# Kernel optimization log

Measured on AMD Instinct MI355X. Metric: run time of the kernel, lower is better.

Reference implementation:

```python
import jax, jax.numpy as jnp
import numpy as np

C = 128      # out_channels
G = 4        # RecConvLayer num_groups
BS, CIN, H, W = 4, 3, 96, 96
GN = 8
EPS = 1e-5


def _conv2d(x, w, b, pad):
    out = jax.lax.conv_general_dilated(
        x, w, (1, 1), [(pad, pad), (pad, pad)],
        dimension_numbers=("NCHW", "OIHW", "NCHW"))
    return out + b[None, :, None, None]


def _prelu(x, a):
    return jnp.maximum(x, 0) + a[0] * jnp.minimum(x, 0)


def _group_norm(x, w, b):
    bs, c, h, wd = x.shape
    xg = x.reshape(bs, GN, c // GN, h, wd)
    mu = xg.mean(axis=(2, 3, 4), keepdims=True)
    var = xg.var(axis=(2, 3, 4), keepdims=True)  # biased, as torch GroupNorm
    xn = ((xg - mu) * jax.lax.rsqrt(var + EPS)).reshape(bs, c, h, wd)
    return xn * w[None, :, None, None] + b[None, :, None, None]


def _single_conv(x, w, b, a, gw, gb, pad):
    # SingleConvLayer in eval mode: Conv2d -> PReLU -> GroupNorm (no noise)
    return _group_norm(_prelu(_conv2d(x, w, b, pad), a), gw, gb)


def _bidir_gru_layer(x, wih, whh, bih, bhh):
    # x: (T,B,Din); wih: (2,3C,Din); whh: (2,3C,C); bih/bhh: (2,3C)
    Cc = whh.shape[-1]
    h0 = jnp.zeros((x.shape[1], Cc), x.dtype)

    def run_dir(gx, wh, bh):
        def step(h, g):
            gh = h @ wh.T + bh
            r = jax.nn.sigmoid(g[:, :Cc] + gh[:, :Cc])
            z = jax.nn.sigmoid(g[:, Cc:2 * Cc] + gh[:, Cc:2 * Cc])
            n = jnp.tanh(g[:, 2 * Cc:] + r * gh[:, 2 * Cc:])
            hn = (1.0 - z) * n + z * h
            return hn, hn
        return jax.lax.scan(step, h0, gx)[1]

    yf = run_dir(x @ wih[0].T + bih[0], whh[0], bhh[0])
    yb = run_dir(x[::-1] @ wih[1].T + bih[1], whh[1], bhh[1])[::-1]
    return jnp.concatenate([yf, yb], axis=-1)  # (T,B,2C)


def _gru2(x, wih0, whh0, bih0, bhh0, wih1, whh1, bih1, bhh1):
    y = _bidir_gru_layer(x, wih0, whh0, bih0, bhh0)
    return _bidir_gru_layer(y, wih1, whh1, bih1, bhh1)


_gru_groups = jax.vmap(_gru2, in_axes=(1, 0, 0, 0, 0, 0, 0, 0, 0), out_axes=1)


def _run_gru(x_tgbc, p):
    out = _gru_groups(x_tgbc, *p)               # (T,G,B,2C)
    t, g, b, _ = out.shape
    return out.reshape(t, g, b, 2, -1).mean(axis=3)  # mean over directions -> (T,G,B,C)


def _forward(x, conv1_w, conv1_b, prelu1_a, gn1_w, gn1_b,
             conv2_w, conv2_b, prelu2_a, gn2_w, gn2_b,
             comb_w, comb_b, prelu3_a, gn3_w, gn3_b,
             h_wih0, h_whh0, h_bih0, h_bhh0, h_wih1, h_whh1, h_bih1, h_bhh1,
             v_wih0, v_whh0, v_bih0, v_bhh0, v_wih1, v_whh1, v_bih1, v_bhh1,
             h1_wih0, h1_whh0, h1_bih0, h1_bhh0, h1_wih1, h1_whh1, h1_bih1, h1_bhh1,
             v1_wih0, v1_whh0, v1_bih0, v1_bhh0, v1_wih1, v1_whh1, v1_bih1, v1_bhh1):
    x = _single_conv(x, conv1_w, conv1_b, prelu1_a, gn1_w, gn1_b, 1)
    x = _single_conv(x, conv2_w, conv2_b, prelu2_a, gn2_w, gn2_b, 1)
    bs, c, m, n = x.shape
    vg, hg = n // G, m // G
    y = jnp.transpose(x, (0, 3, 2, 1))                               # (bs,n,m,c)
    y1 = jnp.transpose(y.reshape(bs, G, vg * m, c), (2, 1, 0, 3))    # vertical seqs (m*vg,G,bs,c)
    ym = jnp.transpose(y, (0, 2, 1, 3))                              # (bs,m,n,c)
    y2 = jnp.transpose(ym.reshape(bs, G, hg * n, c), (2, 1, 0, 3))   # horizontal seqs (n*hg,G,bs,c)

    hn = _run_gru(y2, (h_wih0, h_whh0, h_bih0, h_bhh0, h_wih1, h_whh1, h_bih1, h_bhh1))
    vn = _run_gru(y1, (v_wih0, v_whh0, v_bih0, v_bhh0, v_wih1, v_whh1, v_bih1, v_bhh1))

    hn_b = jnp.transpose(hn, (2, 1, 0, 3)).reshape(bs, m, n, c)
    y1b = jnp.transpose(jnp.transpose(hn_b, (0, 2, 1, 3)).reshape(bs, G, vg * m, c), (2, 1, 0, 3))
    vn_b = jnp.transpose(vn, (2, 1, 0, 3)).reshape(bs, n, m, c)
    y2b = jnp.transpose(jnp.transpose(vn_b, (0, 2, 1, 3)).reshape(bs, G, hg * n, c), (2, 1, 0, 3))

    hn2 = _run_gru(y2b, (h1_wih0, h1_whh0, h1_bih0, h1_bhh0, h1_wih1, h1_whh1, h1_bih1, h1_bhh1))
    vn2 = _run_gru(y1b, (v1_wih0, v1_whh0, v1_bih0, v1_bhh0, v1_wih1, v1_whh1, v1_bih1, v1_bhh1))

    hcnm = jnp.transpose(jnp.transpose(hn2, (2, 1, 0, 3)).reshape(bs, m, n, c), (0, 3, 1, 2))  # (bs,c,m,n)
    vcnm = jnp.transpose(jnp.transpose(vn2, (2, 1, 0, 3)).reshape(bs, n, m, c), (0, 3, 2, 1))  # (bs,c,m,n)
    return _single_conv(jnp.concatenate([hcnm, vcnm], axis=1), comb_w, comb_b, prelu3_a, gn3_w, gn3_b, 0)


def setup_inputs() -> dict:
    key = jax.random.key(0)
    ks = jax.random.split(key, 8)
    nrm = lambda k, s, sc: jax.random.normal(k, s, jnp.float32) * sc
    inp = {
        "x": nrm(ks[0], (BS, CIN, H, W), 1.0),
        "conv1_w": nrm(ks[1], (C, CIN, 3, 3), 0.1), "conv1_b": nrm(ks[2], (C,), 0.05),
        "prelu1_a": jnp.full((1,), 0.25, jnp.float32),
        "gn1_w": jnp.ones((C,), jnp.float32), "gn1_b": jnp.zeros((C,), jnp.float32),
        "conv2_w": nrm(ks[3], (C, C, 3, 3), 0.03), "conv2_b": nrm(ks[4], (C,), 0.05),
        "prelu2_a": jnp.full((1,), 0.25, jnp.float32),
        "gn2_w": jnp.ones((C,), jnp.float32), "gn2_b": jnp.zeros((C,), jnp.float32),
        "comb_w": nrm(ks[5], (C, 2 * C, 1, 1), 0.05), "comb_b": nrm(ks[6], (C,), 0.05),
        "prelu3_a": jnp.full((1,), 0.25, jnp.float32),
        "gn3_w": jnp.ones((C,), jnp.float32), "gn3_b": jnp.zeros((C,), jnp.float32),
    }
    shapes = [("wih0", (G, 2, 3 * C, C)), ("whh0", (G, 2, 3 * C, C)),
              ("bih0", (G, 2, 3 * C)), ("bhh0", (G, 2, 3 * C)),
              ("wih1", (G, 2, 3 * C, 2 * C)), ("whh1", (G, 2, 3 * C, C)),
              ("bih1", (G, 2, 3 * C)), ("bhh1", (G, 2, 3 * C))]
    for i, p in enumerate(["h", "v", "h1", "v1"]):
        kp = jax.random.split(jax.random.fold_in(key, 100 + i), 8)
        for j, (nm, sh) in enumerate(shapes):
            inp[p + "_" + nm] = nrm(kp[j], sh, 0.05)
    return inp


def reference(x, conv1_w, conv1_b, prelu1_a, gn1_w, gn1_b,
              conv2_w, conv2_b, prelu2_a, gn2_w, gn2_b,
              comb_w, comb_b, prelu3_a, gn3_w, gn3_b,
              h_wih0, h_whh0, h_bih0, h_bhh0, h_wih1, h_whh1, h_bih1, h_bhh1,
              v_wih0, v_whh0, v_bih0, v_bhh0, v_wih1, v_whh1, v_bih1, v_bhh1,
              h1_wih0, h1_whh0, h1_bih0, h1_bhh0, h1_wih1, h1_whh1, h1_bih1, h1_bhh1,
              v1_wih0, v1_whh0, v1_bih0, v1_bhh0, v1_wih1, v1_whh1, v1_bih1, v1_bhh1):
    return _forward(x, conv1_w, conv1_b, prelu1_a, gn1_w, gn1_b,
                    conv2_w, conv2_b, prelu2_a, gn2_w, gn2_b,
                    comb_w, comb_b, prelu3_a, gn3_w, gn3_b,
                    h_wih0, h_whh0, h_bih0, h_bhh0, h_wih1, h_whh1, h_bih1, h_bhh1,
                    v_wih0, v_whh0, v_bih0, v_bhh0, v_wih1, v_whh1, v_bih1, v_bhh1,
                    h1_wih0, h1_whh0, h1_bih0, h1_bhh0, h1_wih1, h1_whh1, h1_bih1, h1_bhh1,
                    v1_wih0, v1_whh0, v1_bih0, v1_bhh0, v1_wih1, v1_whh1, v1_bih1, v1_bhh1)
```

## Files before the change

kernel.cpp:

```cpp
#include <hip/hip_runtime.h>

typedef unsigned short u16;
typedef __attribute__((ext_vector_type(8))) short bf16x8;
typedef __attribute__((ext_vector_type(4))) float f32x4;
typedef __attribute__((ext_vector_type(4))) int   i32x4;

#define DEVFN static __device__ __forceinline__
#define AS_G __attribute__((address_space(1)))
#define AS_L __attribute__((address_space(3)))

DEVFN float b2f(u16 u){ return __uint_as_float(((unsigned int)u)<<16); }
DEVFN u16 f2b(float f){ unsigned int x = __float_as_uint(f); x += 0x7FFFu + ((x>>16)&1u); return (u16)(x>>16); }
DEVFN float fastrcp(float x){ return __builtin_amdgcn_rcpf(x); }

struct CastArgs { const float* s[8]; u16* d[8]; int n[8]; };
__global__ void castf2b_g(CastArgs a)
{
    int p = blockIdx.y;
    int i = blockIdx.x*256 + threadIdx.x;
    if (i < a.n[p]) a.d[p][i] = f2b(a.s[p][i]);
}

struct QuantArgs { const float* w[8]; char* q[8]; float* dq[8]; };
__global__ void quant_whh_g(QuantArgs a)
{
    int p = blockIdx.y;
    int row = blockIdx.x;
    int lane = threadIdx.x;
    const float* wr = a.w[p] + (long long)row*128;
    float v0 = wr[lane], v1 = wr[lane+64];
    float m = fmaxf(fabsf(v0), fabsf(v1));
#pragma unroll
    for (int off = 32; off; off >>= 1) m = fmaxf(m, __shfl_xor(m, off));
    float s = (m > 0.f) ? m * (1.f/127.f) : 1.f;
    float inv = 1.f / s;
    a.q[p][(long long)row*128 + lane]      = (char)__float2int_rn(v0 * inv);
    a.q[p][(long long)row*128 + lane + 64] = (char)__float2int_rn(v1 * inv);
    if (lane == 0) a.dq[p][row] = s * (1.f/127.f);
}

__global__ __launch_bounds__(256)
void gemm_bt(const u16* __restrict__ A, const u16* __restrict__ B,
             const float* __restrict__ bias, u16* __restrict__ C,
             int K, int N,
             long long zA, long long zB, long long zBias, long long zC,
             const float* __restrict__ alphaP, float* __restrict__ stats, int rowsPerB)
{
    __shared__ __align__(16) u16 As[128*32];
    __shared__ __align__(16) u16 Bs[128*32];
    __shared__ float sstat[16];

    const int tid  = threadIdx.x;
    const int wave = tid >> 6, lane = tid & 63;
    const int quad = lane >> 4, l16 = lane & 15;
    const int wm = wave & 1, wn = wave >> 1;
    const long long z = blockIdx.z;
    A += z * zA; B += z * zB; C += z * zC;
    if (bias) bias += z * zBias;
    const int lin   = blockIdx.y * gridDim.x + blockIdx.x;
    const int mBase = (int)(lin / gridDim.y) * 128;
    const int nBase = (int)(lin % gridDim.y) * 128;

    f32x4 acc[4][4];
#pragma unroll
    for (int i = 0; i < 4; i++)
#pragma unroll
        for (int j = 0; j < 4; j++) acc[i][j] = (f32x4){0.f,0.f,0.f,0.f};

    const int srow = lane >> 2;
    const int sk   = (lane & 3) * 8;
    const int nK = K >> 5;

    for (int kk = 0; kk < nK; ++kk) {
        const int k0 = kk << 5;
#pragma unroll
        for (int q = 0; q < 2; q++) {
            const u16* ga = A + (long long)(mBase + wave*32 + q*16 + srow) * K + k0 + sk;
            const u16* gb = B + (long long)(nBase + wave*32 + q*16 + srow) * K + k0 + sk;
            __builtin_amdgcn_global_load_lds((const AS_G unsigned int*)ga,
                (AS_L unsigned int*)(As + (wave*32 + q*16)*32), 16, 0, 0);
            __builtin_amdgcn_global_load_lds((const AS_G unsigned int*)gb,
                (AS_L unsigned int*)(Bs + (wave*32 + q*16)*32), 16, 0, 0);
        }
        __syncthreads();
        bf16x8 af[4], bfr[4];
#pragma unroll
        for (int mt = 0; mt < 4; mt++) af[mt]  = *(const bf16x8*)(As + (wm*64 + mt*16 + l16)*32 + quad*8);
#pragma unroll
        for (int nt = 0; nt < 4; nt++) bfr[nt] = *(const bf16x8*)(Bs + (wn*64 + nt*16 + l16)*32 + quad*8);
#pragma unroll
        for (int mt = 0; mt < 4; mt++)
#pragma unroll
            for (int nt = 0; nt < 4; nt++)
                acc[mt][nt] = __builtin_amdgcn_mfma_f32_16x16x32_bf16(af[mt], bfr[nt], acc[mt][nt], 0, 0, 0);
        __syncthreads();
    }

    const bool doStats = (stats != nullptr);
    const float alpha = alphaP ? alphaP[0] : 0.f;
    if (doStats) { if (tid < 16) sstat[tid] = 0.f; __syncthreads(); }

    float lsum[4] = {0,0,0,0}, lsq[4] = {0,0,0,0};
#pragma unroll
    for (int nt = 0; nt < 4; nt++) {
        const int col = nBase + wn*64 + nt*16 + l16;
        const float bv = bias ? bias[col] : 0.f;
#pragma unroll
        for (int mt = 0; mt < 4; mt++) {
#pragma unroll
            for (int r = 0; r < 4; r++) {
                const int row = mBase + wm*64 + mt*16 + quad*4 + r;
                float v = acc[mt][nt][r] + bv;
                if (alphaP) v = v > 0.f ? v : alpha * v;
                C[(long long)row * N + col] = f2b(v);
                lsum[nt] += v; lsq[nt] += v * v;
            }
        }
    }
    if (doStats) {
#pragma unroll
        for (int nt = 0; nt < 4; nt++) {
            const int gn = wn*4 + nt;
            atomicAdd(&sstat[gn], lsum[nt]);
            atomicAdd(&sstat[8 + gn], lsq[nt]);
        }
        __syncthreads();
        if (tid < 16) {
            const int b = mBase / rowsPerB;
            atomicAdd(&stats[b*16 + tid], sstat[tid]);
        }
    }
}

#define HSB 144
#define BURST 16
#define NCHUNK 16
#define CHUNK  144
#define WARM   112

__global__ __launch_bounds__(512, 2)
void gru_rec(const u16* __restrict__ gxH, const u16* __restrict__ gxV,
             const char* __restrict__ qwH, const char* __restrict__ qwV,
             const float* __restrict__ dqH, const float* __restrict__ dqV,
             const float* __restrict__ bhhH, const float* __restrict__ bhhV,
             u16* __restrict__ outH, u16* __restrict__ outV)
{
    const int id    = blockIdx.x / NCHUNK;
    const int chunk = blockIdx.x % NCHUNK;
    const int stack = id >> 3, g = (id >> 1) & 3, d = id & 1;
    const u16*  gx  = (stack ? gxV : gxH) + (long long)g*9216*768 + d*384;
    const char* qw  = (stack ? qwV : qwH) + (long long)(g*2 + d)*384*128;
    const float* dqv = (stack ? dqV : dqH) + (g*2 + d)*384;
    const float* bhh = (stack ? bhhV : bhhH) + (g*2 + d)*384;
    u16* out = (stack ? outV : outH) + (long long)g*9216*256 + d*128;

    const int sBegin = chunk * CHUNK;
    const int sEnd   = sBegin + CHUNK;
    const int sw     = (chunk == 0) ? 0 : sBegin - WARM;

    const int tid = threadIdx.x;
    const int w = tid >> 6, lane = tid & 63;
    const int quad = lane >> 4, l16 = lane & 15;

    __shared__ __align__(16) char hbf8[2][16*HSB];
    __shared__ __align__(16) u16 outs[2][BURST*512];
    for (int i = tid; i < 2*16*HSB; i += 512) ((char*)hbf8)[i] = 0;

    const int col = w*16 + l16;
    i32x4 ifrag[3][2];
#pragma unroll
    for (int gate = 0; gate < 3; ++gate)
#pragma unroll
        for (int kc = 0; kc < 2; ++kc)
            ifrag[gate][kc] = *(const i32x4*)(qw + (long long)(gate*128 + col)*128 + kc*64 + quad*16);

    const float dqR = dqv[col], dqZ = dqv[128 + col], dqN = dqv[256 + col];
    const float bhr = bhh[col], bhz = bhh[128 + col], bhn = bhh[256 + col];
    float h = 0.f;

    const int step = d ? -1 : 1;
    const int t0 = d ? 2303 : 0;
    const long long rowStride = (long long)step * 3072;

    u16 bankA[BURST][3], bankB[BURST][3];
    const i32x4 zi = {0,0,0,0};

    auto loadBank = [&](u16 (&bk)[BURST][3], int sbase) {
        if (sbase >= sEnd) return;
        const u16* p = gx + (long long)((t0 + step*sbase)*4 + quad)*768 + col;
#pragma unroll
        for (int j = 0; j < BURST; j++) {
            bk[j][0] = p[0]; bk[j][1] = p[128]; bk[j][2] = p[256];
            p += rowStride;
        }
    };

    auto flushOut = [&](int sbase, int bank) {
        const u16* ob = outs[bank];
#pragma unroll
        for (int c = 0; c < 2; c++) {
            const int lin = (tid + c*512) * 8;
            const int s   = lin >> 9;
            const int rem = lin & 511;
            const int q   = rem >> 7, cc = rem & 127;
            const int tt  = t0 + step * (sbase + s);
            *(uint4*)(out + (long long)(tt*4 + q)*256 + cc) = *(const uint4*)(ob + lin);
        }
    };

    auto stepf = [&](int j, int bank, u16 g0, u16 g1, u16 g2) {
        const char* hb = hbf8[j & 1];
        char* hw = (char*)hbf8[(j + 1) & 1];
        i32x4 a0 = *(const i32x4*)(hb + l16*HSB + quad*16);
        i32x4 a1 = *(const i32x4*)(hb + l16*HSB + 64 + quad*16);
        i32x4 aR = __builtin_amdgcn_mfma_i32_16x16x64_i8(a0, ifrag[0][0], zi, 0, 0, 0);
        i32x4 aZ = __builtin_amdgcn_mfma_i32_16x16x64_i8(a0, ifrag[1][0], zi, 0, 0, 0);
        i32x4 aN = __builtin_amdgcn_mfma_i32_16x16x64_i8(a0, ifrag[2][0], zi, 0, 0, 0);
        aR = __builtin_amdgcn_mfma_i32_16x16x64_i8(a1, ifrag[0][1], aR, 0, 0, 0);
        aZ = __builtin_amdgcn_mfma_i32_16x16x64_i8(a1, ifrag[1][1], aZ, 0, 0, 0);
        aN = __builtin_amdgcn_mfma_i32_16x16x64_i8(a1, ifrag[2][1], aN, 0, 0, 0);
        float r  = fastrcp(1.f + __expf(-(b2f(g0) + bhr + (float)aR[0] * dqR)));
        float zz = fastrcp(1.f + __expf(-(b2f(g1) + bhz + (float)aZ[0] * dqZ)));
        float nn = b2f(g2) + r * ((float)aN[0] * dqN + bhn);
        nn = 1.f - 2.f * fastrcp(__expf(2.f * nn) + 1.f);
        h = zz * (h - nn) + nn;
        hw[4*quad*HSB + col] = (char)__float2int_rn(h * 127.f);
        outs[bank][j*512 + quad*128 + col] = f2b(h);
        __syncthreads();
    };

    loadBank(bankA, sw);
    __syncthreads();

    for (int base = sw; base < sEnd; base += 2*BURST) {
        loadBank(bankB, base + BURST);
#pragma unroll
        for (int j = 0; j < BURST; j++) stepf(j, 0, bankA[j][0], bankA[j][1], bankA[j][2]);
        if (base >= sBegin) flushOut(base, 0);
        loadBank(bankA, base + 2*BURST);
#pragma unroll
        for (int j = 0; j < BURST; j++) stepf(j, 1, bankB[j][0], bankB[j][1], bankB[j][2]);
        const int b2s = base + BURST;
        if (b2s >= sBegin && b2s < sEnd) flushOut(b2s, 1);
    }
}

__global__ void repack_w(const float* __restrict__ w1, const float* __restrict__ w2,
                         const float* __restrict__ wc,
                         u16* __restrict__ w1r, u16* __restrict__ w2r, u16* __restrict__ wcr)
{
    int idx = blockIdx.x*256 + threadIdx.x;
    if (idx < 128*1152) {
        int o = idx / 1152, k = idx % 1152, tap = k >> 7, ci = k & 127;
        w2r[idx] = f2b(w2[(o*128 + ci)*9 + tap]);
    }
    if (idx < 128*32) {
        int o = idx >> 5, k = idx & 31;
        float v = 0.f;
        if (k < 27) { int tap = k/3, ci = k - tap*3; v = w1[(o*3 + ci)*9 + tap]; }
        w1r[idx] = f2b(v);
    }
    if (idx < 128*256) wcr[idx] = f2b(wc[idx]);
}

__global__ void im2col1(const float* __restrict__ x, u16* __restrict__ A1)
{
    int row = blockIdx.x*256 + threadIdx.x;
    if (row >= 36864) return;
    int b = row / 9216, rem = row % 9216, m = rem / 96, n = rem % 96;
    u16* dst = A1 + (long long)row*32;
#pragma unroll
    for (int k = 0; k < 32; k++) {
        float v = 0.f;
        if (k < 27) {
            int tap = k/3, ci = k - tap*3;
            int mm = m + tap/3 - 1, nn = n + tap%3 - 1;
            if (mm >= 0 && mm < 96 && nn >= 0 && nn < 96)
                v = x[((b*3 + ci)*96 + mm)*96 + nn];
        }
        dst[k] = f2b(v);
    }
}

__global__ void make_ss(const float* __restrict__ stats, const float* __restrict__ gw,
                        const float* __restrict__ gb, float* __restrict__ sc,
                        float* __restrict__ sh, float invCnt)
{
    int idx = blockIdx.x*256 + threadIdx.x;
    if (idx >= 512) return;
    int b = idx >> 7, c = idx & 127, gn = c >> 4;
    float s = stats[b*16 + gn], q = stats[b*16 + 8 + gn];
    float mu = s * invCnt, var = fmaxf(q * invCnt - mu*mu, 0.f);
    float rstd = rsqrtf(var + 1e-5f);
    float scale = rstd * gw[c];
    sc[idx] = scale;
    sh[idx] = gb[c] - mu * scale;
}

__global__ void im2col2(const u16* __restrict__ buf1, const float* __restrict__ sc,
                        const float* __restrict__ sh, u16* __restrict__ A2)
{
    int idx = blockIdx.x*256 + threadIdx.x;
    int row = idx / 144, q = idx % 144;
    int tap = q >> 4, ci0 = (q & 15) << 3;
    int b = row / 9216, rem = row % 9216, m = rem / 96, n = rem % 96;
    int mm = m + tap/3 - 1, nn = n + tap%3 - 1;
    bf16x8 o = (bf16x8){0,0,0,0,0,0,0,0};
    if (mm >= 0 && mm < 96 && nn >= 0 && nn < 96) {
        bf16x8 v = *(const bf16x8*)(buf1 + (long long)(b*9216 + mm*96 + nn)*128 + ci0);
#pragma unroll
        for (int j = 0; j < 8; j++)
            o[j] = (short)f2b(b2f((u16)v[j]) * sc[b*128 + ci0 + j] + sh[b*128 + ci0 + j]);
    }
    *(bf16x8*)(A2 + (long long)row*1152 + tap*128 + ci0) = o;
}

__global__ void repack_seq(const u16* __restrict__ buf2, const float* __restrict__ sc,
                           const float* __restrict__ sh, u16* __restrict__ xh, u16* __restrict__ xv)
{
    int idx = blockIdx.x*256 + threadIdx.x;
    int c0 = (idx & 15) << 3, r1 = idx >> 4;
    int b = r1 & 3, r2 = r1 >> 2;
    int t = r2 % 2304, g = r2 / 2304;
    int iw = t / 96, pos = t % 96;
    int rowH = b*9216 + (g*24 + iw)*96 + pos;
    int rowV = b*9216 + pos*96 + (g*24 + iw);
    bf16x8 vh = *(const bf16x8*)(buf2 + (long long)rowH*128 + c0);
    bf16x8 vv = *(const bf16x8*)(buf2 + (long long)rowV*128 + c0);
    bf16x8 oh, ov;
#pragma unroll
    for (int j = 0; j < 8; j++) {
        float scale = sc[b*128 + c0 + j], shift = sh[b*128 + c0 + j];
        oh[j] = (short)f2b(b2f((u16)vh[j]) * scale + shift);
        ov[j] = (short)f2b(b2f((u16)vv[j]) * scale + shift);
    }
    *(bf16x8*)(xh + ((long long)r1 << 7) + c0) = oh;
    *(bf16x8*)(xv + ((long long)r1 << 7) + c0) = ov;
}

__global__ void repack_B(const u16* __restrict__ z1H, const u16* __restrict__ z1V,
                         u16* __restrict__ xh2, u16* __restrict__ xv2)
{
    int idx = blockIdx.x*256 + threadIdx.x;
    int c0 = (idx & 15) << 3, r1 = idx >> 4;
    int b = r1 & 3, r2 = r1 >> 2;
    int t = r2 % 2304, g = r2 / 2304;
    {
        int ih2 = t / 96, n = t % 96, gs = n / 24, iv = n % 24;
        long long s = ((long long)gs*9216 + (iv*96 + g*24 + ih2)*4 + b)*256 + c0;
        bf16x8 a = *(const bf16x8*)(z1V + s);
        bf16x8 bb = *(const bf16x8*)(z1V + s + 128);
        bf16x8 o;
#pragma unroll
        for (int j = 0; j < 8; j++) o[j] = (short)f2b(0.5f*(b2f((u16)a[j]) + b2f((u16)bb[j])));
        *(bf16x8*)(xh2 + ((long long)r1 << 7) + c0) = o;
    }
    {
        int iv = t / 96, m = t % 96, gs = m / 24, ih = m % 24;
        long long s = ((long long)gs*9216 + (ih*96 + g*24 + iv)*4 + b)*256 + c0;
        bf16x8 a = *(const bf16x8*)(z1H + s);
        bf16x8 bb = *(const bf16x8*)(z1H + s + 128);
        bf16x8 o;
#pragma unroll
        for (int j = 0; j < 8; j++) o[j] = (short)f2b(0.5f*(b2f((u16)a[j]) + b2f((u16)bb[j])));
        *(bf16x8*)(xv2 + ((long long)r1 << 7) + c0) = o;
    }
}

__global__ void repack_comb(const u16* __restrict__ z1H, const u16* __restrict__ z1V,
                            u16* __restrict__ Ac)
{
    int idx = blockIdx.x*256 + threadIdx.x;
    int k0 = (idx & 31) << 3;
    int row = idx >> 5;
    int b = row / 9216, rem = row % 9216, m = rem / 96, n = rem % 96;
    const u16* src;
    long long s;
    if (k0 < 128) {
        int g = m / 24, ih = m % 24, ts = ih*96 + n;
        s = ((long long)g*9216 + ts*4 + b)*256 + k0;
        src = z1H;
    } else {
        int c = k0 - 128, g = n / 24, iv = n % 24, ts = iv*96 + m;
        s = ((long long)g*9216 + ts*4 + b)*256 + c;
        src = z1V;
    }
    bf16x8 a = *(const bf16x8*)(src + s);
    bf16x8 bb = *(const bf16x8*)(src + s + 128);
    bf16x8 o;
#pragma unroll
    for (int j = 0; j < 8; j++) o[j] = (short)f2b(0.5f*(b2f((u16)a[j]) + b2f((u16)bb[j])));
    *(bf16x8*)(Ac + (long long)row*256 + k0) = o;
}

__global__ void final_kernel(const u16* __restrict__ p3, const float* __restrict__ sc,
                             const float* __restrict__ sh, float* __restrict__ out)
{
    __shared__ float tile[128*97];
    int bm = blockIdx.x;
    int b = bm / 96, m = bm % 96;
    int tid = threadIdx.x;
    int rowbase = b*9216 + m*96;
    for (int idx = tid; idx < 96*128; idx += 256) {
        int n = idx >> 7, o = idx & 127;
        float v = b2f(p3[(long long)(rowbase + n)*128 + o]);
        tile[o*97 + n] = v * sc[b*128 + o] + sh[b*128 + o];
    }
    __syncthreads();
    for (int idx = tid; idx < 96*128; idx += 256) {
        int o = idx / 96, n = idx % 96;
        out[((long long)(b*128 + o)*96 + m)*96 + n] = tile[o*97 + n];
    }
}

extern "C" void kernel_launch(void* const* d_in, const int* in_sizes, int n_in,
                              void* d_out, int out_size, void* d_ws, size_t ws_size,
                              hipStream_t stream)
{
    (void)in_sizes; (void)n_in; (void)out_size;
    auto F = [&](int i){ return (const float*)d_in[i]; };

    char* ws = (char*)d_ws;
    size_t off = 0;
    auto alloc = [&](size_t bytes)->char* {
        char* p = ws + off;
        off += (bytes + 255) & ~(size_t)255;
        return p;
    };

    float* stats = (float*)alloc(3*64*sizeof(float));
    float* sc1 = (float*)alloc(512*4); float* sh1 = (float*)alloc(512*4);
    float* sc2 = (float*)alloc(512*4); float* sh2 = (float*)alloc(512*4);
    float* sc3 = (float*)alloc(512*4); float* sh3 = (float*)alloc(512*4);
    u16* w1r  = (u16*)alloc((size_t)128*32*2);
    u16* w2r  = (u16*)alloc((size_t)128*1152*2);
    u16* wcr  = (u16*)alloc((size_t)128*256*2);
    u16 *wih0c[4], *wih1c[4];
    char *qw0[4], *qw1[4];
    float *dq0[4], *dq1[4];
    for (int p = 0; p < 4; p++) {
        wih0c[p] = (u16*)alloc((size_t)393216*2);
        wih1c[p] = (u16*)alloc((size_t)786432*2);
        qw0[p]   = (char*)alloc((size_t)393216);
        qw1[p]   = (char*)alloc((size_t)393216);
        dq0[p]   = (float*)alloc((size_t)3072*4);
        dq1[p]   = (float*)alloc((size_t)3072*4);
    }
    u16* A1   = (u16*)alloc((size_t)36864*32*2);
    u16* buf1 = (u16*)alloc((size_t)36864*128*2);
    u16* buf2 = (u16*)alloc((size_t)36864*128*2);
    u16* xh   = (u16*)alloc((size_t)4718592*2);
    u16* xv   = (u16*)alloc((size_t)4718592*2);
    u16* gxH  = (u16*)alloc((size_t)4*9216*768*2);
    u16* gxV  = (u16*)alloc((size_t)4*9216*768*2);
    u16* z1H  = (u16*)alloc((size_t)4*9216*256*2);
    u16* z1V  = (u16*)alloc((size_t)4*9216*256*2);

    u16* A2  = gxH;
    u16* y0H = xh;
    u16* y0V = buf1;
    u16* Ac  = xh;
    u16* p3  = buf1;

    if (ws_size < off) return;

    hipMemsetAsync(stats, 0, 3*64*sizeof(float), stream);
    repack_w<<<576, 256, 0, stream>>>(F(1), F(6), F(11), w1r, w2r, wcr);
    im2col1<<<144, 256, 0, stream>>>(F(0), A1);

    CastArgs ca;
    QuantArgs qa;
    for (int p = 0; p < 4; p++) {
        int base = 16 + p*8;
        ca.s[p]   = F(base+0); ca.d[p]   = wih0c[p]; ca.n[p]   = 393216;
        ca.s[p+4] = F(base+4); ca.d[p+4] = wih1c[p]; ca.n[p+4] = 786432;
        qa.w[p]   = F(base+1); qa.q[p]   = qw0[p];   qa.dq[p]   = dq0[p];
        qa.w[p+4] = F(base+5); qa.q[p+4] = qw1[p];   qa.dq[p+4] = dq1[p];
    }
    castf2b_g<<<dim3(3072, 8), 256, 0, stream>>>(ca);
    quant_whh_g<<<dim3(3072, 8), 64, 0, stream>>>(qa);

    gemm_bt<<<dim3(288,1,1), 256, 0, stream>>>(A1, w1r, F(2), buf1, 32, 128,
        0,0,0,0, F(3), stats + 0, 9216);
    make_ss<<<2, 256, 0, stream>>>(stats + 0, F(4), F(5), sc1, sh1, 1.f/147456.f);

    im2col2<<<20736, 256, 0, stream>>>(buf1, sc1, sh1, A2);
    gemm_bt<<<dim3(288,1,1), 256, 0, stream>>>(A2, w2r, F(7), buf2, 1152, 128,
        0,0,0,0, F(8), stats + 64, 9216);
    make_ss<<<2, 256, 0, stream>>>(stats + 64, F(9), F(10), sc2, sh2, 1.f/147456.f);

    repack_seq<<<2304, 256, 0, stream>>>(buf2, sc2, sh2, xh, xv);

    const long long zA0 = 9216LL*128, zA1 = 9216LL*256;
    const long long zB0 = 768LL*128,  zB1 = 768LL*256;
    const long long zC  = 9216LL*768;

    gemm_bt<<<dim3(72,6,4), 256, 0, stream>>>(xh, wih0c[0], F(18), gxH, 128, 768, zA0, zB0, 768, zC, nullptr, nullptr, 0);
    gemm_bt<<<dim3(72,6,4), 256, 0, stream>>>(xv, wih0c[1], F(26), gxV, 128, 768, zA0, zB0, 768, zC, nullptr, nullptr, 0);
    gru_rec<<<16*NCHUNK, 512, 0, stream>>>(gxH, gxV, qw0[0], qw0[1], dq0[0], dq0[1], F(19), F(27), y0H, y0V);
    gemm_bt<<<dim3(72,6,4), 256, 0, stream>>>(y0H, wih1c[0], F(22), gxH, 256, 768, zA1, zB1, 768, zC, nullptr, nullptr, 0);
    gemm_bt<<<dim3(72,6,4), 256, 0, stream>>>(y0V, wih1c[1], F(30), gxV, 256, 768, zA1, zB1, 768, zC, nullptr, nullptr, 0);
    gru_rec<<<16*NCHUNK, 512, 0, stream>>>(gxH, gxV, qw1[0], qw1[1], dq1[0], dq1[1], F(23), F(31), z1H, z1V);

    repack_B<<<2304, 256, 0, stream>>>(z1H, z1V, xh, xv);
    gemm_bt<<<dim3(72,6,4), 256, 0, stream>>>(xh, wih0c[2], F(34), gxH, 128, 768, zA0, zB0, 768, zC, nullptr, nullptr, 0);
    gemm_bt<<<dim3(72,6,4), 256, 0, stream>>>(xv, wih0c[3], F(42), gxV, 128, 768, zA0, zB0, 768, zC, nullptr, nullptr, 0);
    gru_rec<<<16*NCHUNK, 512, 0, stream>>>(gxH, gxV, qw0[2], qw0[3], dq0[2], dq0[3], F(35), F(43), y0H, y0V);
    gemm_bt<<<dim3(72,6,4), 256, 0, stream>>>(y0H, wih1c[2], F(38), gxH, 256, 768, zA1, zB1, 768, zC, nullptr, nullptr, 0);
    gemm_bt<<<dim3(72,6,4), 256, 0, stream>>>(y0V, wih1c[3], F(46), gxV, 256, 768, zA1, zB1, 768, zC, nullptr, nullptr, 0);
    gru_rec<<<16*NCHUNK, 512, 0, stream>>>(gxH, gxV, qw1[2], qw1[3], dq1[2], dq1[3], F(39), F(47), z1H, z1V);

    repack_comb<<<4608, 256, 0, stream>>>(z1H, z1V, Ac);
    gemm_bt<<<dim3(288,1,1), 256, 0, stream>>>(Ac, wcr, F(12), p3, 256, 128,
        0,0,0,0, F(13), stats + 128, 9216);
    make_ss<<<2, 256, 0, stream>>>(stats + 128, F(14), F(15), sc3, sh3, 1.f/147456.f);
    final_kernel<<<384, 256, 0, stream>>>(p3, sc3, sh3, (float*)d_out);
}
```

Measured before the change: 973.7 us.

## Merge H/V input GEMMs into one launch, transpose MFMA for vector stores, lighter barrier

The paired horizontal and vertical GRU input-projection GEMMs are merged into one launch with twice the z-dimension, selecting operand pointers by z. The MFMA operand order is swapped so each lane holds four consecutive columns, letting the epilogue do one float4 bias load and packed 8-byte bf16 stores instead of scalar stores. In the GRU recurrence, __syncthreads is replaced by an inline-asm LDS waitcnt plus s_barrier, which does not wait on outstanding global memory operations. Together these aim to cut launch overhead, scattered epilogue stores, and barrier stalls on pending global traffic.

```diff
diff --git a/kernel.cpp b/kernel.cpp
--- a/kernel.cpp
+++ b/kernel.cpp
@@ -44,7 +44,9 @@
              const float* __restrict__ bias, u16* __restrict__ C,
              int K, int N,
              long long zA, long long zB, long long zBias, long long zC,
-             const float* __restrict__ alphaP, float* __restrict__ stats, int rowsPerB)
+             const float* __restrict__ alphaP, float* __restrict__ stats, int rowsPerB,
+             const u16* __restrict__ Ax, const u16* __restrict__ Bx,
+             const float* __restrict__ biasx, u16* __restrict__ Cx, int zHalf)
 {
     __shared__ __align__(16) u16 As[128*32];
     __shared__ __align__(16) u16 Bs[128*32];
@@ -54,9 +56,13 @@
     const int wave = tid >> 6, lane = tid & 63;
     const int quad = lane >> 4, l16 = lane & 15;
     const int wm = wave & 1, wn = wave >> 1;
-    const long long z = blockIdx.z;
-    A += z * zA; B += z * zB; C += z * zC;
-    if (bias) bias += z * zBias;
+
+    long long z = blockIdx.z;
+    const u16* Ap = A; const u16* Bp = B; const float* bp = bias; u16* Cp = C;
+    if (Ax && z >= zHalf) { Ap = Ax; Bp = Bx; bp = biasx; Cp = Cx; z -= zHalf; }
+    Ap += z * zA; Bp += z * zB; Cp += z * zC;
+    if (bp) bp += z * zBias;
+
     const int lin   = blockIdx.y * gridDim.x + blockIdx.x;
     const int mBase = (int)(lin / gridDim.y) * 128;
     const int nBase = (int)(lin % gridDim.y) * 128;
@@ -75,8 +81,8 @@
         const int k0 = kk << 5;
 #pragma unroll
         for (int q = 0; q < 2; q++) {
-            const u16* ga = A + (long long)(mBase + wave*32 + q*16 + srow) * K + k0 + sk;
-            const u16* gb = B + (long long)(nBase + wave*32 + q*16 + srow) * K + k0 + sk;
+            const u16* ga = Ap + (long long)(mBase + wave*32 + q*16 + srow) * K + k0 + sk;
+            const u16* gb = Bp + (long long)(nBase + wave*32 + q*16 + srow) * K + k0 + sk;
             __builtin_amdgcn_global_load_lds((const AS_G unsigned int*)ga,
                 (AS_L unsigned int*)(As + (wave*32 + q*16)*32), 16, 0, 0);
             __builtin_amdgcn_global_load_lds((const AS_G unsigned int*)gb,
@@ -92,7 +98,7 @@
         for (int mt = 0; mt < 4; mt++)
 #pragma unroll
             for (int nt = 0; nt < 4; nt++)
-                acc[mt][nt] = __builtin_amdgcn_mfma_f32_16x16x32_bf16(af[mt], bfr[nt], acc[mt][nt], 0, 0, 0);
+                acc[mt][nt] = __builtin_amdgcn_mfma_f32_16x16x32_bf16(bfr[nt], af[mt], acc[mt][nt], 0, 0, 0);
         __syncthreads();
     }
 
@@ -103,18 +109,30 @@
     float lsum[4] = {0,0,0,0}, lsq[4] = {0,0,0,0};
 #pragma unroll
     for (int nt = 0; nt < 4; nt++) {
-        const int col = nBase + wn*64 + nt*16 + l16;
-        const float bv = bias ? bias[col] : 0.f;
+        const int col0 = nBase + wn*64 + nt*16 + quad*4;
+        float4 bv4 = {0.f, 0.f, 0.f, 0.f};
+        if (bp) bv4 = *(const float4*)(bp + col0);
 #pragma unroll
         for (int mt = 0; mt < 4; mt++) {
-#pragma unroll
-            for (int r = 0; r < 4; r++) {
-                const int row = mBase + wm*64 + mt*16 + quad*4 + r;
-                float v = acc[mt][nt][r] + bv;
-                if (alphaP) v = v > 0.f ? v : alpha * v;
-                C[(long long)row * N + col] = f2b(v);
-                lsum[nt] += v; lsq[nt] += v * v;
+            const int row = mBase + wm*64 + mt*16 + l16;
+            float v0 = acc[mt][nt][0] + bv4.x;
+            float v1 = acc[mt][nt][1] + bv4.y;
+            float v2 = acc[mt][nt][2] + bv4.z;
+            float v3 = acc[mt][nt][3] + bv4.w;
+            if (alphaP) {
+                v0 = v0 > 0.f ? v0 : alpha * v0;
+                v1 = v1 > 0.f ? v1 : alpha * v1;
+                v2 = v2 > 0.f ? v2 : alpha * v2;
+                v3 = v3 > 0.f ? v3 : alpha * v3;
             }
+            if (doStats) {
+                lsum[nt] += v0 + v1 + v2 + v3;
+                lsq[nt]  += v0*v0 + v1*v1 + v2*v2 + v3*v3;
+            }
+            uint2 pk;
+            pk.x = (unsigned)f2b(v0) | ((unsigned)f2b(v1) << 16);
+            pk.y = (unsigned)f2b(v2) | ((unsigned)f2b(v3) << 16);
+            *(uint2*)(Cp + (long long)row * N + col0) = pk;
         }
     }
     if (doStats) {
@@ -206,6 +224,10 @@
             const int tt  = t0 + step * (sbase + s);
             *(uint4*)(out + (long long)(tt*4 + q)*256 + cc) = *(const uint4*)(ob + lin);
         }
+    };
+
+    auto ldsbar = [&]() {
+        asm volatile("s_waitcnt lgkmcnt(0)\n\ts_barrier" ::: "memory");
     };
 
     auto stepf = [&](int j, int bank, u16 g0, u16 g1, u16 g2) {
@@ -226,7 +248,7 @@
         h = zz * (h - nn) + nn;
         hw[4*quad*HSB + col] = (char)__float2int_rn(h * 127.f);
         outs[bank][j*512 + quad*128 + col] = f2b(h);
-        __syncthreads();
+        ldsbar();
     };
 
     loadBank(bankA, sw);
@@ -481,12 +503,12 @@
     quant_whh_g<<<dim3(3072, 8), 64, 0, stream>>>(qa);
 
     gemm_bt<<<dim3(288,1,1), 256, 0, stream>>>(A1, w1r, F(2), buf1, 32, 128,
-        0,0,0,0, F(3), stats + 0, 9216);
+        0,0,0,0, F(3), stats + 0, 9216, nullptr, nullptr, nullptr, nullptr, 0);
     make_ss<<<2, 256, 0, stream>>>(stats + 0, F(4), F(5), sc1, sh1, 1.f/147456.f);
 
     im2col2<<<20736, 256, 0, stream>>>(buf1, sc1, sh1, A2);
     gemm_bt<<<dim3(288,1,1), 256, 0, stream>>>(A2, w2r, F(7), buf2, 1152, 128,
-        0,0,0,0, F(8), stats + 64, 9216);
+        0,0,0,0, F(8), stats + 64, 9216, nullptr, nullptr, nullptr, nullptr, 0);
     make_ss<<<2, 256, 0, stream>>>(stats + 64, F(9), F(10), sc2, sh2, 1.f/147456.f);
 
     repack_seq<<<2304, 256, 0, stream>>>(buf2, sc2, sh2, xh, xv);
@@ -495,24 +517,24 @@
     const long long zB0 = 768LL*128,  zB1 = 768LL*256;
     const long long zC  = 9216LL*768;
 
-    gemm_bt<<<dim3(72,6,4), 256, 0, stream>>>(xh, wih0c[0], F(18), gxH, 128, 768, zA0, zB0, 768, zC, nullptr, nullptr, 0);
-    gemm_bt<<<dim3(72,6,4), 256, 0, stream>>>(xv, wih0c[1], F(26), gxV, 128, 768, zA0, zB0, 768, zC, nullptr, nullptr, 0);
+    gemm_bt<<<dim3(72,6,8), 256, 0, stream>>>(xh, wih0c[0], F(18), gxH, 128, 768, zA0, zB0, 768, zC,
+        nullptr, nullptr, 0, xv, wih0c[1], F(26), gxV, 4);
     gru_rec<<<16*NCHUNK, 512, 0, stream>>>(gxH, gxV, qw0[0], qw0[1], dq0[0], dq0[1], F(19), F(27), y0H, y0V);
-    gemm_bt<<<dim3(72,6,4), 256, 0, stream>>>(y0H, wih1c[0], F(22), gxH, 256, 768, zA1, zB1, 768, zC, nullptr, nullptr, 0);
-    gemm_bt<<<dim3(72,6,4), 256, 0, stream>>>(y0V, wih1c[1], F(30), gxV, 256, 768, zA1, zB1, 768, zC, nullptr, nullptr, 0);
+    gemm_bt<<<dim3(72,6,8), 256, 0, stream>>>(y0H, wih1c[0], F(22), gxH, 256, 768, zA1, zB1, 768, zC,
+        nullptr, nullptr, 0, y0V, wih1c[1], F(30), gxV, 4);
     gru_rec<<<16*NCHUNK, 512, 0, stream>>>(gxH, gxV, qw1[0], qw1[1], dq1[0], dq1[1], F(23), F(31), z1H, z1V);
 
     repack_B<<<2304, 256, 0, stream>>>(z1H, z1V, xh, xv);
-    gemm_bt<<<dim3(72,6,4), 256, 0, stream>>>(xh, wih0c[2], F(34), gxH, 128, 768, zA0, zB0, 768, zC, nullptr, nullptr, 0);
-    gemm_bt<<<dim3(72,6,4), 256, 0, stream>>>(xv, wih0c[3], F(42), gxV, 128, 768, zA0, zB0, 768, zC, nullptr, nullptr, 0);
+    gemm_bt<<<dim3(72,6,8), 256, 0, stream>>>(xh, wih0c[2], F(34), gxH, 128, 768, zA0, zB0, 768, zC,
+        nullptr, nullptr, 0, xv, wih0c[3], F(42), gxV, 4);
     gru_rec<<<16*NCHUNK, 512, 0, stream>>>(gxH, gxV, qw0[2], qw0[3], dq0[2], dq0[3], F(35), F(43), y0H, y0V);
-    gemm_bt<<<dim3(72,6,4), 256, 0, stream>>>(y0H, wih1c[2], F(38), gxH, 256, 768, zA1, zB1, 768, zC, nullptr, nullptr, 0);
-    gemm_bt<<<dim3(72,6,4), 256, 0, stream>>>(y0V, wih1c[3], F(46), gxV, 256, 768, zA1, zB1, 768, zC, nullptr, nullptr, 0);
+    gemm_bt<<<dim3(72,6,8), 256, 0, stream>>>(y0H, wih1c[2], F(38), gxH, 256, 768, zA1, zB1, 768, zC,
+        nullptr, nullptr, 0, y0V, wih1c[3], F(46), gxV, 4);
     gru_rec<<<16*NCHUNK, 512, 0, stream>>>(gxH, gxV, qw1[2], qw1[3], dq1[2], dq1[3], F(39), F(47), z1H, z1V);
 
     repack_comb<<<4608, 256, 0, stream>>>(z1H, z1V, Ac);
     gemm_bt<<<dim3(288,1,1), 256, 0, stream>>>(Ac, wcr, F(12), p3, 256, 128,
-        0,0,0,0, F(13), stats + 128, 9216);
+        0,0,0,0, F(13), stats + 128, 9216, nullptr, nullptr, nullptr, nullptr, 0);
     make_ss<<<2, 256, 0, stream>>>(stats + 128, F(14), F(15), sc3, sh3, 1.f/147456.f);
     final_kernel<<<384, 256, 0, stream>>>(p3, sc3, sh3, (float*)d_out);
 }
```

After: 961.4 us. About the same (-1.3%).
